# Optimization experiments

Measured on AMD Instinct MI355X. Metric: run time of the kernel, lower is better.

The kernel has to match this reference:

```python
import jax, jax.numpy as jnp
import numpy as np

B, V, D = 8, 1024, 512
H = 8
HD = D // H
MAX_HOP = 8


def setup_inputs() -> dict:
    key = jax.random.key(0)
    ks = jax.random.split(key, 5)
    x = jax.random.normal(ks[0], (B, V, D), dtype=jnp.float32)
    w_qkv = jax.random.normal(ks[1], (D, 3 * D), dtype=jnp.float32) * (D ** -0.5)
    w_out = jax.random.normal(ks[2], (D, D), dtype=jnp.float32) * (D ** -0.5)
    b_out = jnp.zeros((D,), dtype=jnp.float32)
    rpe_bias = jax.random.normal(ks[3], (H, MAX_HOP + 1), dtype=jnp.float32) * 0.02
    hop_matrix = jax.random.randint(ks[4], (V, V), 0, MAX_HOP + 1, dtype=jnp.int32)
    return {"x": x, "w_qkv": w_qkv, "w_out": w_out, "b_out": b_out,
            "rpe_bias": rpe_bias, "hop_matrix": hop_matrix}


def reference(x, w_qkv, w_out, b_out, rpe_bias, hop_matrix):
    b, v, d = x.shape
    scale = HD ** -0.5
    qkv = x @ w_qkv                                   # [B, V, 3D]
    q, k, val = jnp.split(qkv, 3, axis=-1)
    # [B, V, D] -> [B, H, V, HD]
    def split_heads(t):
        return t.reshape(b, v, H, HD).transpose(0, 2, 1, 3)
    q, k, val = split_heads(q), split_heads(k), split_heads(val)
    scores = jnp.einsum('bhvd,bhwd->bhvw', q, k)      # [B, H, V, V]
    bias = rpe_bias[:, hop_matrix]                    # gather -> [H, V, V]
    attn = jax.nn.softmax((scores + bias[None]) * scale, axis=-1)
    out_heads = jnp.einsum('bhvw,bhwd->bhvd', attn, val)
    out = out_heads.transpose(0, 2, 1, 3).reshape(b, v, d)
    out = out @ w_out + b_out
    return out, attn
```

## Files before the change

### kernel.cpp

```cpp
#include <hip/hip_runtime.h>

typedef __attribute__((ext_vector_type(8))) short bf16x8;
typedef __attribute__((ext_vector_type(4))) float f32x4;

#define MFMA16(A,B,C) __builtin_amdgcn_mfma_f32_16x16x32_bf16(A,B,C,0,0,0)

__device__ __forceinline__ unsigned short f2bf(float f){
  unsigned int u = __float_as_uint(f);
  u += 0x7FFFu + ((u >> 16) & 1u);
  return (unsigned short)(u >> 16);
}
__device__ __forceinline__ float bf2f(unsigned short s){
  return __uint_as_float(((unsigned int)s) << 16);
}
__device__ __forceinline__ int swz(int row, int kbyte){
  return (row * 128 + kbyte) ^ ((row & 7) << 4);
}

__global__ __launch_bounds__(256) void k_prep(
    const float* __restrict__ w_qkv, const float* __restrict__ w_out,
    unsigned short* __restrict__ wqT, unsigned short* __restrict__ woT)
{
  int idx = blockIdx.x * 256 + threadIdx.x;
  if (idx < 1536 * 512) {
    int n = idx >> 9, kq = idx & 511;
    wqT[idx] = f2bf(w_qkv[(size_t)kq * 1536 + n]);
  } else {
    int j = idx - 1536 * 512;
    int n = j >> 9, kq = j & 511;
    woT[j] = f2bf(w_out[(size_t)kq * 512 + n]);
  }
}

__global__ __launch_bounds__(256) void k_bias(
    const int* __restrict__ hop, const float* __restrict__ rpe_bias,
    unsigned short* __restrict__ biasT)
{
  __shared__ float rl[72];
  const int tid = threadIdx.x;
  if (tid < 72) rl[tid] = rpe_bias[tid];
  __syncthreads();
  const int idx = blockIdx.x * 256 + tid;
  const int hv = hop[idx];
#pragma unroll
  for (int h = 0; h < 8; ++h)
    biasT[((size_t)h << 20) + idx] = f2bf(rl[h * 9 + hv]);
}

__global__ __launch_bounds__(256) void k_qkv(
    const float* __restrict__ x, const unsigned short* __restrict__ wqT,
    unsigned short* __restrict__ q, unsigned short* __restrict__ k_,
    unsigned short* __restrict__ valT)
{
  __shared__ char lds[32768];
  char* At = lds; char* Bt = lds + 16384;
  const int tid = threadIdx.x;
  const int wid = tid >> 6, lane = tid & 63, g = lane >> 4, r = lane & 15;
  const int wm = wid >> 1, wn = wid & 1;
  const int m0 = blockIdx.x * 128, n0 = blockIdx.y * 128;

  f32x4 acc[4][4];
#pragma unroll
  for (int a = 0; a < 4; ++a)
#pragma unroll
    for (int b = 0; b < 4; ++b) acc[a][b] = (f32x4){0.f, 0.f, 0.f, 0.f};

  for (int kt = 0; kt < 8; ++kt) {
    const int k0 = kt * 64;
    __syncthreads();
#pragma unroll
    for (int it = 0; it < 8; ++it) {
      int c = tid + it * 256;
      int row = c >> 4, c4 = c & 15;
      float4 xv = *reinterpret_cast<const float4*>(x + (size_t)(m0 + row) * 512 + k0 + c4 * 4);
      uint2 hv;
      hv.x = (unsigned)f2bf(xv.x) | ((unsigned)f2bf(xv.y) << 16);
      hv.y = (unsigned)f2bf(xv.z) | ((unsigned)f2bf(xv.w) << 16);
      *reinterpret_cast<uint2*>(At + swz(row, c4 * 8)) = hv;
    }
#pragma unroll
    for (int it = 0; it < 4; ++it) {
      int c = tid + it * 256;
      int row = c >> 3, c8 = c & 7;
      *reinterpret_cast<uint4*>(Bt + swz(row, c8 * 16)) =
          *reinterpret_cast<const uint4*>(wqT + (size_t)(n0 + row) * 512 + k0 + c8 * 8);
    }
    __syncthreads();
#pragma unroll
    for (int kk = 0; kk < 2; ++kk) {
      bf16x8 af[4], bf[4];
      const int kb = (kk * 32 + 8 * g) * 2;
#pragma unroll
      for (int mi = 0; mi < 4; ++mi)
        af[mi] = *reinterpret_cast<const bf16x8*>(At + swz(wm * 64 + mi * 16 + r, kb));
#pragma unroll
      for (int ni = 0; ni < 4; ++ni)
        bf[ni] = *reinterpret_cast<const bf16x8*>(Bt + swz(wn * 64 + ni * 16 + r, kb));
#pragma unroll
      for (int mi = 0; mi < 4; ++mi)
#pragma unroll
        for (int ni = 0; ni < 4; ++ni)
          acc[mi][ni] = MFMA16(af[mi], bf[ni], acc[mi][ni]);
    }
  }
  const int s = n0 >> 9;
#pragma unroll
  for (int mi = 0; mi < 4; ++mi)
#pragma unroll
    for (int ni = 0; ni < 4; ++ni)
#pragma unroll
      for (int i = 0; i < 4; ++i) {
        int m = m0 + wm * 64 + mi * 16 + 4 * g + i;
        int n = n0 + wn * 64 + ni * 16 + r;
        int b = m >> 10, v = m & 1023;
        int cc = n & 511, h = cc >> 6, d = cc & 63;
        int bh = b * 8 + h;
        unsigned short bfv = f2bf(acc[mi][ni][i]);
        if (s == 2)      valT[((size_t)bh * 64 + d) * 1024 + v] = bfv;
        else if (s == 0) q [((size_t)bh * 1024 + v) * 64 + d] = bfv;
        else             k_[((size_t)bh * 1024 + v) * 64 + d] = bfv;
      }
}

__global__ __launch_bounds__(256, 4) void k_attn(
    const unsigned short* __restrict__ q, const unsigned short* __restrict__ k_,
    const unsigned short* __restrict__ valT,
    const unsigned short* __restrict__ biasT,
    float* __restrict__ attn, unsigned short* __restrict__ oh)
{
  __shared__ unsigned short P[16 * 1040];
  __shared__ float red[2][4][16];
  const int tid = threadIdx.x;
  const int wid = tid >> 6, lane = tid & 63, g = lane >> 4, r = lane & 15;
  const int blk = blockIdx.x;
  const int vt = blk & 63, bh = blk >> 6, h = bh & 7;
  const int v0 = vt * 16;

  const unsigned short* bb = biasT + ((size_t)h << 20) + (size_t)v0 * 1024;
#pragma unroll
  for (int it = 0; it < 8; ++it) {
    int e = tid + it * 256;
    int row = e >> 7, c8 = e & 127;
    *reinterpret_cast<uint4*>(&P[row * 1040 + c8 * 8]) =
        *reinterpret_cast<const uint4*>(bb + (size_t)row * 1024 + c8 * 8);
  }

  const unsigned short* qp = q + ((size_t)bh * 1024 + v0) * 64;
  bf16x8 qf[2];
#pragma unroll
  for (int kk = 0; kk < 2; ++kk)
    qf[kk] = *reinterpret_cast<const bf16x8*>(qp + r * 64 + kk * 32 + 8 * g);
  __syncthreads();

  const unsigned short* kb = k_ + (size_t)bh * 65536;
  f32x4 s[16];
#pragma unroll
  for (int ct = 0; ct < 16; ++ct) {
    const int wcol = wid * 256 + ct * 16 + r;
    f32x4 acc = (f32x4){0.f, 0.f, 0.f, 0.f};
#pragma unroll
    for (int kk = 0; kk < 2; ++kk) {
      bf16x8 kf = *reinterpret_cast<const bf16x8*>(kb + (size_t)wcol * 64 + kk * 32 + 8 * g);
      acc = MFMA16(qf[kk], kf, acc);
    }
#pragma unroll
    for (int i = 0; i < 4; ++i)
      s[ct][i] = (acc[i] + bf2f(P[(4 * g + i) * 1040 + wcol])) * 0.125f;
  }

  float mx[4] = {-1e30f, -1e30f, -1e30f, -1e30f};
#pragma unroll
  for (int ct = 0; ct < 16; ++ct)
#pragma unroll
    for (int i = 0; i < 4; ++i) mx[i] = fmaxf(mx[i], s[ct][i]);
#pragma unroll
  for (int o = 1; o <= 8; o <<= 1)
#pragma unroll
    for (int i = 0; i < 4; ++i) mx[i] = fmaxf(mx[i], __shfl_xor(mx[i], o, 64));
  if (r == 0)
#pragma unroll
    for (int i = 0; i < 4; ++i) red[0][wid][4 * g + i] = mx[i];
  __syncthreads();
#pragma unroll
  for (int i = 0; i < 4; ++i) {
    float M = red[0][0][4 * g + i];
#pragma unroll
    for (int w = 1; w < 4; ++w) M = fmaxf(M, red[0][w][4 * g + i]);
    mx[i] = M;
  }

  float sm[4] = {0.f, 0.f, 0.f, 0.f};
#pragma unroll
  for (int ct = 0; ct < 16; ++ct)
#pragma unroll
    for (int i = 0; i < 4; ++i) {
      float e = __expf(s[ct][i] - mx[i]);
      s[ct][i] = e;
      sm[i] += e;
    }
#pragma unroll
  for (int o = 1; o <= 8; o <<= 1)
#pragma unroll
    for (int i = 0; i < 4; ++i) sm[i] += __shfl_xor(sm[i], o, 64);
  if (r == 0)
#pragma unroll
    for (int i = 0; i < 4; ++i) red[1][wid][4 * g + i] = sm[i];
  __syncthreads();
  float inv[4];
#pragma unroll
  for (int i = 0; i < 4; ++i) {
    float T = red[1][0][4 * g + i] + red[1][1][4 * g + i] +
              red[1][2][4 * g + i] + red[1][3][4 * g + i];
    inv[i] = 1.0f / T;
  }

  float* ab = attn + ((size_t)bh * 1024 + v0) * 1024;
#pragma unroll
  for (int ct = 0; ct < 16; ++ct) {
    const int col = wid * 256 + ct * 16 + r;
#pragma unroll
    for (int i = 0; i < 4; ++i) {
      const int row = 4 * g + i;
      float a = s[ct][i] * inv[i];
      __builtin_nontemporal_store(a, ab + (size_t)row * 1024 + col);
      P[row * 1040 + col] = f2bf(a);
    }
  }
  __syncthreads();

  const unsigned short* vT = valT + ((size_t)bh * 64 + wid * 16) * 1024;
  f32x4 a0 = (f32x4){0.f,0.f,0.f,0.f}, a1 = a0, a2 = a0, a3 = a0;
  for (int kc = 0; kc < 32; kc += 4) {
    const int base = r * 1040, vbase = kc * 32 + 8 * g;
    bf16x8 p0 = *reinterpret_cast<const bf16x8*>(&P[base + vbase]);
    bf16x8 p1 = *reinterpret_cast<const bf16x8*>(&P[base + vbase + 32]);
    bf16x8 p2 = *reinterpret_cast<const bf16x8*>(&P[base + vbase + 64]);
    bf16x8 p3 = *reinterpret_cast<const bf16x8*>(&P[base + vbase + 96]);
    bf16x8 v0_ = *reinterpret_cast<const bf16x8*>(vT + (size_t)r * 1024 + vbase);
    bf16x8 v1_ = *reinterpret_cast<const bf16x8*>(vT + (size_t)r * 1024 + vbase + 32);
    bf16x8 v2_ = *reinterpret_cast<const bf16x8*>(vT + (size_t)r * 1024 + vbase + 64);
    bf16x8 v3_ = *reinterpret_cast<const bf16x8*>(vT + (size_t)r * 1024 + vbase + 96);
    a0 = MFMA16(p0, v0_, a0);
    a1 = MFMA16(p1, v1_, a1);
    a2 = MFMA16(p2, v2_, a2);
    a3 = MFMA16(p3, v3_, a3);
  }
  f32x4 acc = (a0 + a1) + (a2 + a3);
  const int b = bh >> 3;
#pragma unroll
  for (int i = 0; i < 4; ++i) {
    size_t oi = ((size_t)(b * 1024 + v0 + 4 * g + i)) * 512 + h * 64 + wid * 16 + r;
    oh[oi] = f2bf(acc[i]);
  }
}

__global__ __launch_bounds__(256) void k_out(
    const unsigned short* __restrict__ oh, const unsigned short* __restrict__ woT,
    const float* __restrict__ b_out, float* __restrict__ out)
{
  __shared__ char lds[32768];
  char* At = lds; char* Bt = lds + 16384;
  const int tid = threadIdx.x;
  const int wid = tid >> 6, lane = tid & 63, g = lane >> 4, r = lane & 15;
  const int wm = wid >> 1, wn = wid & 1;
  const int m0 = blockIdx.x * 128, n0 = blockIdx.y * 128;

  f32x4 acc[4][4];
#pragma unroll
  for (int a = 0; a < 4; ++a)
#pragma unroll
    for (int b = 0; b < 4; ++b) acc[a][b] = (f32x4){0.f, 0.f, 0.f, 0.f};

  for (int kt = 0; kt < 8; ++kt) {
    const int k0 = kt * 64;
    __syncthreads();
#pragma unroll
    for (int it = 0; it < 4; ++it) {
      int c = tid + it * 256;
      int row = c >> 3, c8 = c & 7;
      *reinterpret_cast<uint4*>(At + swz(row, c8 * 16)) =
          *reinterpret_cast<const uint4*>(oh + (size_t)(m0 + row) * 512 + k0 + c8 * 8);
      *reinterpret_cast<uint4*>(Bt + swz(row, c8 * 16)) =
          *reinterpret_cast<const uint4*>(woT + (size_t)(n0 + row) * 512 + k0 + c8 * 8);
    }
    __syncthreads();
#pragma unroll
    for (int kk = 0; kk < 2; ++kk) {
      bf16x8 a4[4], b4[4];
      const int kb = (kk * 32 + 8 * g) * 2;
#pragma unroll
      for (int mi = 0; mi < 4; ++mi)
        a4[mi] = *reinterpret_cast<const bf16x8*>(At + swz(wm * 64 + mi * 16 + r, kb));
#pragma unroll
      for (int ni = 0; ni < 4; ++ni)
        b4[ni] = *reinterpret_cast<const bf16x8*>(Bt + swz(wn * 64 + ni * 16 + r, kb));
#pragma unroll
      for (int mi = 0; mi < 4; ++mi)
#pragma unroll
        for (int ni = 0; ni < 4; ++ni)
          acc[mi][ni] = MFMA16(a4[mi], b4[ni], acc[mi][ni]);
    }
  }
#pragma unroll
  for (int mi = 0; mi < 4; ++mi)
#pragma unroll
    for (int ni = 0; ni < 4; ++ni)
#pragma unroll
      for (int i = 0; i < 4; ++i) {
        int m = m0 + wm * 64 + mi * 16 + 4 * g + i;
        int n = n0 + wn * 64 + ni * 16 + r;
        __builtin_nontemporal_store(acc[mi][ni][i] + b_out[n], out + (size_t)m * 512 + n);
      }
}

extern "C" void kernel_launch(void* const* d_in, const int* in_sizes, int n_in,
                              void* d_out, int out_size, void* d_ws, size_t ws_size,
                              hipStream_t stream) {
  const float *x = nullptr, *w_qkv = nullptr, *w_out = nullptr,
              *b_out = nullptr, *rpe = nullptr;
  const int* hop = nullptr;
  for (int i = 0; i < n_in; ++i) {
    switch (in_sizes[i]) {
      case 4194304: x     = (const float*)d_in[i]; break;
      case 786432:  w_qkv = (const float*)d_in[i]; break;
      case 262144:  w_out = (const float*)d_in[i]; break;
      case 512:     b_out = (const float*)d_in[i]; break;
      case 72:      rpe   = (const float*)d_in[i]; break;
      case 1048576: hop   = (const int*)d_in[i];   break;
    }
  }

  float* out  = (float*)d_out;
  float* attn = out + (size_t)4194304;

  char* ws = (char*)d_ws;
  unsigned short* q_    = (unsigned short*)(ws);
  unsigned short* k_    = (unsigned short*)(ws + (size_t) 8388608);
  unsigned short* valT  = (unsigned short*)(ws + (size_t)16777216);
  unsigned short* oh    = (unsigned short*)(ws + (size_t)25165824);
  unsigned short* wqT   = (unsigned short*)(ws + (size_t)33554432);
  unsigned short* woT   = (unsigned short*)(ws + (size_t)35127296);
  unsigned short* biasT = (unsigned short*)(ws + (size_t)35651584);

  k_prep<<<dim3(4096), dim3(256), 0, stream>>>(w_qkv, w_out, wqT, woT);
  k_bias<<<dim3(4096), dim3(256), 0, stream>>>(hop, rpe, biasT);
  k_qkv<<<dim3(64, 12), dim3(256), 0, stream>>>(x, wqT, q_, k_, valT);
  k_attn<<<dim3(4096), dim3(256), 0, stream>>>(q_, k_, valT, biasT, attn, oh);
  k_out<<<dim3(64, 4), dim3(256), 0, stream>>>(oh, woT, b_out, out);
}
```

Baseline: 216.2 us.

## Process 32 query rows per attention block with 8 waves

The attention kernel now handles 32 query rows per block using 512 threads (two row groups of four waves each), which halves the grid to 2048 blocks. It also shrinks the LDS row stride from 1040 to 1032, and the PV loop runs with two accumulators instead of four. The intent is to cut per-block overhead and amortize the bias tile loading and K/V reads over more rows. In exchange it uses twice the LDS per block (about 66KB), which may lower occupancy, and the stride change may alter LDS bank conflicts.

```diff
diff --git a/kernel.cpp b/kernel.cpp
--- a/kernel.cpp
+++ b/kernel.cpp
@@ -122,30 +122,32 @@
       }
 }
 
-__global__ __launch_bounds__(256, 4) void k_attn(
+#define PSTR 1032
+__global__ __launch_bounds__(512, 4) void k_attn(
     const unsigned short* __restrict__ q, const unsigned short* __restrict__ k_,
     const unsigned short* __restrict__ valT,
     const unsigned short* __restrict__ biasT,
     float* __restrict__ attn, unsigned short* __restrict__ oh)
 {
-  __shared__ unsigned short P[16 * 1040];
-  __shared__ float red[2][4][16];
+  __shared__ unsigned short P[32 * PSTR];
+  __shared__ float red[2][8][16];
   const int tid = threadIdx.x;
   const int wid = tid >> 6, lane = tid & 63, g = lane >> 4, r = lane & 15;
+  const int rg = wid >> 2, cg = wid & 3;
   const int blk = blockIdx.x;
-  const int vt = blk & 63, bh = blk >> 6, h = bh & 7;
-  const int v0 = vt * 16;
+  const int vt = blk & 31, bh = blk >> 5, h = bh & 7;
+  const int v0 = vt * 32;
 
   const unsigned short* bb = biasT + ((size_t)h << 20) + (size_t)v0 * 1024;
 #pragma unroll
   for (int it = 0; it < 8; ++it) {
-    int e = tid + it * 256;
+    int e = tid + it * 512;
     int row = e >> 7, c8 = e & 127;
-    *reinterpret_cast<uint4*>(&P[row * 1040 + c8 * 8]) =
+    *reinterpret_cast<uint4*>(&P[row * PSTR + c8 * 8]) =
         *reinterpret_cast<const uint4*>(bb + (size_t)row * 1024 + c8 * 8);
   }
 
-  const unsigned short* qp = q + ((size_t)bh * 1024 + v0) * 64;
+  const unsigned short* qp = q + ((size_t)bh * 1024 + v0 + rg * 16) * 64;
   bf16x8 qf[2];
 #pragma unroll
   for (int kk = 0; kk < 2; ++kk)
@@ -156,7 +158,7 @@
   f32x4 s[16];
 #pragma unroll
   for (int ct = 0; ct < 16; ++ct) {
-    const int wcol = wid * 256 + ct * 16 + r;
+    const int wcol = cg * 256 + ct * 16 + r;
     f32x4 acc = (f32x4){0.f, 0.f, 0.f, 0.f};
 #pragma unroll
     for (int kk = 0; kk < 2; ++kk) {
@@ -165,7 +167,7 @@
     }
 #pragma unroll
     for (int i = 0; i < 4; ++i)
-      s[ct][i] = (acc[i] + bf2f(P[(4 * g + i) * 1040 + wcol])) * 0.125f;
+      s[ct][i] = (acc[i] + bf2f(P[(rg * 16 + 4 * g + i) * PSTR + wcol])) * 0.125f;
   }
 
   float mx[4] = {-1e30f, -1e30f, -1e30f, -1e30f};
@@ -183,9 +185,9 @@
   __syncthreads();
 #pragma unroll
   for (int i = 0; i < 4; ++i) {
-    float M = red[0][0][4 * g + i];
-#pragma unroll
-    for (int w = 1; w < 4; ++w) M = fmaxf(M, red[0][w][4 * g + i]);
+    float M = red[0][rg * 4][4 * g + i];
+#pragma unroll
+    for (int w = 1; w < 4; ++w) M = fmaxf(M, red[0][rg * 4 + w][4 * g + i]);
     mx[i] = M;
   }
 
@@ -209,47 +211,42 @@
   float inv[4];
 #pragma unroll
   for (int i = 0; i < 4; ++i) {
-    float T = red[1][0][4 * g + i] + red[1][1][4 * g + i] +
-              red[1][2][4 * g + i] + red[1][3][4 * g + i];
+    float T = red[1][rg * 4][4 * g + i] + red[1][rg * 4 + 1][4 * g + i] +
+              red[1][rg * 4 + 2][4 * g + i] + red[1][rg * 4 + 3][4 * g + i];
     inv[i] = 1.0f / T;
   }
 
   float* ab = attn + ((size_t)bh * 1024 + v0) * 1024;
 #pragma unroll
   for (int ct = 0; ct < 16; ++ct) {
-    const int col = wid * 256 + ct * 16 + r;
+    const int col = cg * 256 + ct * 16 + r;
 #pragma unroll
     for (int i = 0; i < 4; ++i) {
-      const int row = 4 * g + i;
+      const int row = rg * 16 + 4 * g + i;
       float a = s[ct][i] * inv[i];
       __builtin_nontemporal_store(a, ab + (size_t)row * 1024 + col);
-      P[row * 1040 + col] = f2bf(a);
-    }
-  }
-  __syncthreads();
-
-  const unsigned short* vT = valT + ((size_t)bh * 64 + wid * 16) * 1024;
-  f32x4 a0 = (f32x4){0.f,0.f,0.f,0.f}, a1 = a0, a2 = a0, a3 = a0;
-  for (int kc = 0; kc < 32; kc += 4) {
-    const int base = r * 1040, vbase = kc * 32 + 8 * g;
+      P[row * PSTR + col] = f2bf(a);
+    }
+  }
+  __syncthreads();
+
+  const unsigned short* vT = valT + ((size_t)bh * 64 + cg * 16) * 1024;
+  f32x4 a0 = (f32x4){0.f,0.f,0.f,0.f}, a1 = a0;
+  for (int kc = 0; kc < 32; kc += 2) {
+    const int base = (rg * 16 + r) * PSTR, vbase = kc * 32 + 8 * g;
     bf16x8 p0 = *reinterpret_cast<const bf16x8*>(&P[base + vbase]);
     bf16x8 p1 = *reinterpret_cast<const bf16x8*>(&P[base + vbase + 32]);
-    bf16x8 p2 = *reinterpret_cast<const bf16x8*>(&P[base + vbase + 64]);
-    bf16x8 p3 = *reinterpret_cast<const bf16x8*>(&P[base + vbase + 96]);
     bf16x8 v0_ = *reinterpret_cast<const bf16x8*>(vT + (size_t)r * 1024 + vbase);
     bf16x8 v1_ = *reinterpret_cast<const bf16x8*>(vT + (size_t)r * 1024 + vbase + 32);
-    bf16x8 v2_ = *reinterpret_cast<const bf16x8*>(vT + (size_t)r * 1024 + vbase + 64);
-    bf16x8 v3_ = *reinterpret_cast<const bf16x8*>(vT + (size_t)r * 1024 + vbase + 96);
     a0 = MFMA16(p0, v0_, a0);
     a1 = MFMA16(p1, v1_, a1);
-    a2 = MFMA16(p2, v2_, a2);
-    a3 = MFMA16(p3, v3_, a3);
-  }
-  f32x4 acc = (a0 + a1) + (a2 + a3);
+  }
+  f32x4 acc = a0 + a1;
   const int b = bh >> 3;
 #pragma unroll
   for (int i = 0; i < 4; ++i) {
-    size_t oi = ((size_t)(b * 1024 + v0 + 4 * g + i)) * 512 + h * 64 + wid * 16 + r;
+    size_t oi = ((size_t)(b * 1024 + v0 + rg * 16 + 4 * g + i)) * 512
+              + h * 64 + cg * 16 + r;
     oh[oi] = f2bf(acc[i]);
   }
 }
@@ -345,6 +342,6 @@
   k_prep<<<dim3(4096), dim3(256), 0, stream>>>(w_qkv, w_out, wqT, woT);
   k_bias<<<dim3(4096), dim3(256), 0, stream>>>(hop, rpe, biasT);
   k_qkv<<<dim3(64, 12), dim3(256), 0, stream>>>(x, wqT, q_, k_, valT);
-  k_attn<<<dim3(4096), dim3(256), 0, stream>>>(q_, k_, valT, biasT, attn, oh);
+  k_attn<<<dim3(2048), dim3(512), 0, stream>>>(q_, k_, valT, biasT, attn, oh);
   k_out<<<dim3(64, 4), dim3(256), 0, stream>>>(oh, woT, b_out, out);
 }
```

Result: slower. 237.5 us (+9.8%).
